# Optimization experiments

Measured on AMD Instinct MI355X. Metric: run time of the kernel, lower is better.

Reference implementation:

```python
import jax, jax.numpy as jnp
import numpy as np

MAX_WAVELENGTH = 10000.0
BIG_NEG = -2.3819763e+38
NUM_KV_HEADS = 8
HEAD_DIM = 128


def _apply_rope(x, positions):
    # x: [B, L, H, D], positions: [B, L]
    d = x.shape[-1]
    freq_exponents = (2.0 / d) * jnp.arange(d // 2, dtype=jnp.float32)
    timescale = MAX_WAVELENGTH ** freq_exponents                      # [D/2]
    radians = positions.astype(jnp.float32)[..., None] / timescale    # [B, L, D/2]
    radians = radians[..., None, :]                                   # [B, L, 1, D/2]
    sin, cos = jnp.sin(radians), jnp.cos(radians)
    x1, x2 = jnp.split(x, 2, axis=-1)
    return jnp.concatenate([x1 * cos - x2 * sin, x2 * cos + x1 * sin], axis=-1)


def setup_inputs() -> dict:
    key = jax.random.key(0)
    ks = jax.random.split(key, 4)
    B, T, D = 2, 2048, 4096
    N, K, H = 32, NUM_KV_HEADS, HEAD_DIM
    x = jax.random.normal(ks[0], (B, T, D), dtype=jnp.float32)
    positions = jnp.broadcast_to(jnp.arange(T, dtype=jnp.int32), (B, T))
    # causal mask [B, 1, T, S]
    attn_mask = jnp.broadcast_to(jnp.tril(jnp.ones((T, T), dtype=bool))[None, None], (B, 1, T, T))
    scale = 1.0 / np.sqrt(D)
    wq = jax.random.normal(ks[1], (N, D, H), dtype=jnp.float32) * scale
    wkv = jax.random.normal(ks[2], (2, K, D, H), dtype=jnp.float32) * scale
    wo = jax.random.normal(ks[3], (N, H, D), dtype=jnp.float32) * (1.0 / np.sqrt(N * H))
    return {"x": x, "positions": positions, "attn_mask": attn_mask,
            "wq": wq, "wkv": wkv, "wo": wo, "decode": 0}


def reference(x, positions, attn_mask, wq, wkv, wo, decode):
    # decode=False (prefill); KV cache path not exercised.
    B, T, D = x.shape
    N, _, H = wq.shape
    K = wkv.shape[1]
    G = N // K

    q = jnp.einsum('BTD,NDH->BTNH', x, wq)        # [B, T, N, H]
    k, v = jnp.einsum('BSD,2KDH->2BSKH', x, wkv)  # each [B, S, K, H]

    q = _apply_rope(q, positions) * (H ** -0.5)
    k = _apply_rope(k, positions)

    q = q.reshape(B, T, K, G, H)                  # 'B T (K G) H -> B T K G H'
    logits = jnp.einsum('BTKGH,BSKH->BKGTS', q, k).astype(jnp.float32)
    masked = jnp.where(attn_mask[:, :, None, :, :], logits, BIG_NEG)
    probs = jax.nn.softmax(masked, axis=-1).astype(k.dtype)
    encoded = jnp.einsum('BKGTS,BSKH->BTKGH', probs, v)
    encoded = encoded.reshape(B, T, N, H)
    return jnp.einsum('BTNH,NHD->BTD', encoded, wo)
```

## Files before the change

kernel.cpp:

```cpp
#include <hip/hip_runtime.h>

typedef short short8  __attribute__((ext_vector_type(8)));
typedef short short4v __attribute__((ext_vector_type(4)));
typedef float f32x4   __attribute__((ext_vector_type(4)));

#define B_   2
#define T_   2048
#define D_   4096
#define N_   32
#define KH_  8
#define H_   128
#define BT_  (B_*T_)
#define NH_  (N_*H_)
#define NTK  64

__device__ __forceinline__ short f2bf(float f) {
    unsigned u = __float_as_uint(f);
    u += 0x7fffu + ((u >> 16) & 1u);
    return (short)(u >> 16);
}

__device__ __forceinline__ void gl_lds16(const short* g, short* l) {
    __builtin_amdgcn_global_load_lds(
        (const __attribute__((address_space(1))) void*)(g),
        (__attribute__((address_space(3))) void*)(l), 16, 0, 0);
}

__global__ __launch_bounds__(256) void cast_x_kernel(const float* __restrict__ in,
                                                     short* __restrict__ out) {
    const size_t i = ((size_t)blockIdx.x * 256 + threadIdx.x) * 8;
    float4 v0 = *reinterpret_cast<const float4*>(in + i);
    float4 v1 = *reinterpret_cast<const float4*>(in + i + 4);
    short8 s;
    s[0] = f2bf(v0.x); s[1] = f2bf(v0.y); s[2] = f2bf(v0.z); s[3] = f2bf(v0.w);
    s[4] = f2bf(v1.x); s[5] = f2bf(v1.y); s[6] = f2bf(v1.z); s[7] = f2bf(v1.w);
    *reinterpret_cast<short8*>(out + i) = s;
}

__global__ void transpose_cast_kernel(const float* __restrict__ in,
                                      short* __restrict__ out, int R, int C) {
    __shared__ float tile[32][33];
    const long long slice = blockIdx.z;
    in  += slice * (long long)R * C;
    out += slice * (long long)R * C;
    const int c0 = blockIdx.x * 32, r0 = blockIdx.y * 32;
    const int tx = threadIdx.x, ty = threadIdx.y;
#pragma unroll
    for (int i = 0; i < 4; i++) {
        int r = r0 + ty + i * 8;
        tile[ty + i * 8][tx] = in[(long long)r * C + c0 + tx];
    }
    __syncthreads();
#pragma unroll
    for (int i = 0; i < 4; i++) {
        int cc = c0 + ty + i * 8;
        out[(long long)cc * R + r0 + tx] = f2bf(tile[tx][ty + i * 8]);
    }
}


#define RD_A(cb, jm) {                                                          \
    const int rr_ = arow0 + (jm) * 16;                                          \
    a[jm][0] = *reinterpret_cast<const short8*>(&lds[cb][0][ah][rr_ * 64 + at0]); \
    a[jm][1] = *reinterpret_cast<const short8*>(&lds[cb][0][ah][rr_ * 64 + at1]); }

#define RD_B(cb, jn, jj) {                                                      \
    const int rb_ = (jn) * 16 + l15;                                            \
    b[jj][0] = *reinterpret_cast<const short8*>(&lds[cb][1][wc][rb_ * 64 + at0]); \
    b[jj][1] = *reinterpret_cast<const short8*>(&lds[cb][1][wc][rb_ * 64 + at1]); }

#define STAGE(ab, G, rowbase, sb, h, kt_) {                                     \
    int kt_c = (kt_); if (kt_c > NTK - 1) kt_c = NTK - 1;                       \
    const short* gsrc_ = (G) + (size_t)((rowbase) + (h) * 128 + srow) * 4096    \
                             + kt_c * 64 + sca * 8;                             \
    gl_lds16(gsrc_,            &lds[sb][ab][h][(2 * w) * 512]);                 \
    gl_lds16(gsrc_ + 8 * 4096, &lds[sb][ab][h][(2 * w) * 512 + 512]); }

#define MFMA_Q(JM0, JN0)                                                        \
    __builtin_amdgcn_s_setprio(1);                                              \
    _Pragma("unroll")                                                           \
    for (int jm_ = 0; jm_ < 2; ++jm_)                                           \
    _Pragma("unroll")                                                           \
    for (int jn_ = 0; jn_ < 4; ++jn_)                                           \
    _Pragma("unroll")                                                           \
    for (int ks_ = 0; ks_ < 2; ++ks_)                                           \
        acc[(JM0) + jm_][(JN0) + jn_] = __builtin_amdgcn_mfma_f32_16x16x32_bf16( \
            a[(JM0) + jm_][ks_], b[jn_][ks_], acc[(JM0) + jm_][(JN0) + jn_], 0, 0, 0); \
    __builtin_amdgcn_s_setprio(0);

#define GEMM8_PRO_AND_LOOP(Ap, Bp, m0, n0)                                      \
    f32x4 acc[4][8];                                                            \
    {const f32x4 z_ = {0.f,0.f,0.f,0.f};                                        \
    _Pragma("unroll") for (int jm_=0;jm_<4;++jm_)                               \
    _Pragma("unroll") for (int jn_=0;jn_<8;++jn_) acc[jm_][jn_]=z_;}            \
    short8 a[4][2], b[4][2];                                                    \
    STAGE(0, Ap, m0, 0, 0, 0); STAGE(0, Ap, m0, 0, 1, 0);                       \
    STAGE(1, Bp, n0, 0, 0, 0); STAGE(1, Bp, n0, 0, 1, 0);                       \
    STAGE(0, Ap, m0, 1, 0, 1); STAGE(0, Ap, m0, 1, 1, 1);                       \
    for (int i = 0; i < NTK / 2; ++i) {                                         \
        _Pragma("unroll")                                                       \
        for (int hf = 0; hf < 2; ++hf) {                                        \
            const int cb = hf, sbB = hf ^ 1;                                    \
            const int tB = 2 * i + 1 + hf;                                      \
            const int tA = 2 * i + 2 + hf;                                      \
                                                                        \
            asm volatile("s_waitcnt vmcnt(4)" ::: "memory");                    \
            __builtin_amdgcn_s_barrier();                                       \
            RD_A(cb, 0); RD_A(cb, 1);                                           \
            RD_B(cb, 0, 0); RD_B(cb, 1, 1); RD_B(cb, 2, 2); RD_B(cb, 3, 3);     \
            STAGE(1, Bp, n0, sbB, 0, tB);                                       \
            MFMA_Q(0, 0);                                                       \
                                                                        \
            __builtin_amdgcn_s_barrier();                                       \
            RD_A(cb, 2); RD_A(cb, 3);                                           \
            STAGE(1, Bp, n0, sbB, 1, tB);                                       \
            MFMA_Q(2, 0);                                                       \
                                                                        \
            __builtin_amdgcn_s_barrier();                                       \
            RD_B(cb, 4, 0); RD_B(cb, 5, 1); RD_B(cb, 6, 2); RD_B(cb, 7, 3);     \
            STAGE(0, Ap, m0, hf, 0, tA);                                        \
            MFMA_Q(2, 4);                                                       \
                                                                        \
            __builtin_amdgcn_s_barrier();                                       \
            STAGE(0, Ap, m0, hf, 1, tA);                                        \
            MFMA_Q(0, 4);                                                       \
        }                                                                       \
    }                                                                           \
    asm volatile("s_waitcnt vmcnt(0)" ::: "memory");

__global__ __launch_bounds__(512, 2) void qkv_gemm8_kernel(
    const short* __restrict__ xb, const int* __restrict__ positions,
    const short* __restrict__ wqt,
    short* __restrict__ qo, short* __restrict__ ko, short* __restrict__ vto)
{
    __shared__ short lds[2][2][2][8192];
    const int tid = threadIdx.x;
    const int w = tid >> 6, lane = tid & 63;
    const int quad = lane >> 4, l15 = lane & 15;
    const int wr = w >> 1, wc = w & 1;
    const int ah = wr >> 1;
    const int arow0 = (wr & 1) * 64 + l15;
    const int sw = l15 & 7;
    const int at0 = (quad ^ sw) * 8;
    const int at1 = ((4 + quad) ^ sw) * 8;
    const int srow = 16 * w + (lane >> 3);
    const int sca = (lane & 7) ^ (lane >> 3);
    const int m0 = blockIdx.y * 256;
    const int n0 = blockIdx.x * 256;

    GEMM8_PRO_AND_LOOP(xb, wqt, m0, n0)

    const int head = 2 * blockIdx.x + wc;
    if (head < 40) {
        const float qs = (head < 32) ? (0.08838834764831845f * 1.4426950408889634f) : 1.0f;
#pragma unroll
        for (int jm = 0; jm < 4; ++jm) {
#pragma unroll
            for (int reg = 0; reg < 4; ++reg) {
                const int bt = m0 + wr * 64 + jm * 16 + quad * 4 + reg;
                const int bb = bt >> 11, t = bt & (T_ - 1);
                short* dst = (head < 32)
                    ? qo + ((size_t)(bb * N_ + head) * T_ + t) * H_
                    : ko + ((size_t)(bb * KH_ + (head - 32)) * T_ + t) * H_;
                const float pos = (float)positions[bt];
#pragma unroll
                for (int jn = 0; jn < 4; ++jn) {
                    const int h2 = jn * 16 + l15;
                    float inv_ts = exp2f((float)h2 * -0.20762050593048935f);
                    float rev = pos * inv_ts * 0.15915494309189535f;
                    rev -= floorf(rev);
                    float sn, cs;
                    __sincosf(rev * 6.283185307179586f, &sn, &cs);
                    float x1 = acc[jm][jn][reg], x2 = acc[jm][jn + 4][reg];
                    dst[h2]      = f2bf((x1 * cs - x2 * sn) * qs);
                    dst[h2 + 64] = f2bf((x2 * cs + x1 * sn) * qs);
                }
            }
        }
    } else {
        const int vh = head - 40;
        const int bb = m0 >> 11;
        const int tl0 = (m0 & (T_ - 1)) + wr * 64;
#pragma unroll
        for (int jm = 0; jm < 4; ++jm) {
            const int t0r = tl0 + jm * 16 + quad * 4;
#pragma unroll
            for (int jn = 0; jn < 8; ++jn) {
                const int h = jn * 16 + l15;
                short4v pv;
                pv[0] = f2bf(acc[jm][jn][0]); pv[1] = f2bf(acc[jm][jn][1]);
                pv[2] = f2bf(acc[jm][jn][2]); pv[3] = f2bf(acc[jm][jn][3]);
                *reinterpret_cast<short4v*>(vto + ((size_t)(bb * KH_ + vh) * H_ + h) * T_ + t0r) = pv;
            }
        }
    }
}

__global__ __launch_bounds__(512, 2) void out_gemm8_kernel(
    const short* __restrict__ enc, const short* __restrict__ wot,
    float* __restrict__ out)
{
    __shared__ short lds[2][2][2][8192];
    const int tid = threadIdx.x;
    const int w = tid >> 6, lane = tid & 63;
    const int quad = lane >> 4, l15 = lane & 15;
    const int wr = w >> 1, wc = w & 1;
    const int ah = wr >> 1;
    const int arow0 = (wr & 1) * 64 + l15;
    const int sw = l15 & 7;
    const int at0 = (quad ^ sw) * 8;
    const int at1 = ((4 + quad) ^ sw) * 8;
    const int srow = 16 * w + (lane >> 3);
    const int sca = (lane & 7) ^ (lane >> 3);
    const int m0 = blockIdx.y * 256;
    const int n0 = blockIdx.x * 256;

    GEMM8_PRO_AND_LOOP(enc, wot, m0, n0)

#pragma unroll
    for (int jm = 0; jm < 4; ++jm)
#pragma unroll
        for (int jn = 0; jn < 8; ++jn)
#pragma unroll
            for (int reg = 0; reg < 4; ++reg) {
                const int r = m0 + wr * 64 + jm * 16 + quad * 4 + reg;
                out[(size_t)r * D_ + n0 + wc * 128 + jn * 16 + l15] = acc[jm][jn][reg];
            }
}

__global__ __launch_bounds__(256) void attn_kernel(
    const short* __restrict__ qp, const short* __restrict__ kp,
    const short* __restrict__ vtp, short* __restrict__ encp)
{
    __shared__ short ldsP[4 * 32 * 128];
    const int tid = threadIdx.x;
    const int w = tid >> 6, lane = tid & 63;
    const int quad = lane >> 4, l15 = lane & 15;
    const int widx = blockIdx.x * 4 + w;
    const int pr = widx & 31;
    const int n  = (widx >> 5) & 31;
    const int b  = widx >> 10;
    const int kh = n >> 2;
    short* P = ldsP + w * (32 * 128);

    const short* qbase = qp  + (size_t)(b * N_  + n)  * T_ * H_;
    const short* kbase = kp  + (size_t)(b * KH_ + kh) * T_ * H_;
    const short* vbase = vtp + (size_t)(b * KH_ + kh) * H_ * T_;

    const f32x4 zero4 = {0.f, 0.f, 0.f, 0.f};

    for (int half = 0; half < 2; half++) {
        const int wt = half ? pr : (63 - pr);
        const int t0 = wt * 32;

        short8 qf[2][4];
#pragma unroll
        for (int jc = 0; jc < 2; jc++)
#pragma unroll
            for (int ks = 0; ks < 4; ks++)
                qf[jc][ks] = *reinterpret_cast<const short8*>(
                    qbase + (size_t)(t0 + 16 * jc + l15) * H_ + ks * 32 + quad * 8);

        f32x4 o[2][8];
#pragma unroll
        for (int jm = 0; jm < 2; jm++)
#pragma unroll
            for (int jn = 0; jn < 8; jn++) o[jm][jn] = zero4;
        float lsum[2] = {0.f, 0.f};

        short8 kb[8];
        short8 vb[8];
#pragma unroll
        for (int jn = 0; jn < 8; jn++)
            vb[jn] = *reinterpret_cast<const short8*>(
                vbase + (size_t)(16 * jn + l15) * T_ + quad * 8);
#pragma unroll
        for (int ks = 0; ks < 4; ks++)
#pragma unroll
            for (int jr = 0; jr < 2; jr++)
                kb[2 * ks + jr] = *reinterpret_cast<const short8*>(
                    kbase + (size_t)(16 * jr + l15) * H_ + ks * 32 + quad * 8);

        for (int ss = 0; ss <= wt; ss++) {
            const int s0 = ss * 32;
            const int slot = (ss & 3) * 4;
            const int s0n = (ss < wt) ? s0 + 32 : 0;

            f32x4 s[2][2];
#pragma unroll
            for (int jr = 0; jr < 2; jr++)
#pragma unroll
                for (int jc = 0; jc < 2; jc++) s[jr][jc] = zero4;
#pragma unroll
            for (int ks = 0; ks < 4; ks++)
#pragma unroll
                for (int jr = 0; jr < 2; jr++)
#pragma unroll
                    for (int jc = 0; jc < 2; jc++)
                        s[jr][jc] = __builtin_amdgcn_mfma_f32_16x16x32_bf16(kb[2 * ks + jr], qf[jc][ks], s[jr][jc], 0, 0, 0);

#pragma unroll
            for (int ks = 0; ks < 4; ks++)
#pragma unroll
                for (int jr = 0; jr < 2; jr++)
                    kb[2 * ks + jr] = *reinterpret_cast<const short8*>(
                        kbase + (size_t)(s0n + 16 * jr + l15) * H_ + ks * 32 + quad * 8);

            if (ss == wt) {
#pragma unroll
                for (int jr = 0; jr < 2; jr++)
#pragma unroll
                    for (int jc = 0; jc < 2; jc++)
#pragma unroll
                        for (int reg = 0; reg < 4; reg++) {
                            int sl = 16 * jr + 4 * quad + reg;
                            int tl = 16 * jc + l15;
                            if (sl > tl) s[jr][jc][reg] = -1.0e30f;
                        }
            }

#pragma unroll
            for (int jr = 0; jr < 2; jr++)
#pragma unroll
                for (int jc = 0; jc < 2; jc++) {
                    short4v pk;
#pragma unroll
                    for (int reg = 0; reg < 4; reg++) {
                        float p = exp2f(s[jr][jc][reg]);
                        lsum[jc] += p;
                        pk[reg] = f2bf(p);
                    }
                    const int row = 16 * jc + l15;
                    const int cc  = slot + 2 * jr + (quad >> 1);
                    const int hf  = quad & 1;
                    *reinterpret_cast<short4v*>(
                        &P[row * 128 + ((cc ^ l15) << 3) + (hf << 2)]) = pk;
                }
            asm volatile("s_waitcnt lgkmcnt(0)" ::: "memory");

#pragma unroll
            for (int jm = 0; jm < 2; jm++) {
                short8 pa = *reinterpret_cast<const short8*>(
                    &P[(16 * jm + l15) * 128 + (((slot + quad) ^ l15) << 3)]);
#pragma unroll
                for (int jn = 0; jn < 8; jn++)
                    o[jm][jn] = __builtin_amdgcn_mfma_f32_16x16x32_bf16(pa, vb[jn], o[jm][jn], 0, 0, 0);
            }

#pragma unroll
            for (int jn = 0; jn < 8; jn++)
                vb[jn] = *reinterpret_cast<const short8*>(
                    vbase + (size_t)(16 * jn + l15) * T_ + s0n + quad * 8);
        }

#pragma unroll
        for (int jc = 0; jc < 2; jc++) {
            lsum[jc] += __shfl_xor(lsum[jc], 16, 64);
            lsum[jc] += __shfl_xor(lsum[jc], 32, 64);
        }
#pragma unroll
        for (int jm = 0; jm < 2; jm++)
#pragma unroll
            for (int reg = 0; reg < 4; reg++) {
                const float inv = 1.0f / __shfl(lsum[jm], 4 * quad + reg, 64);
                const int t = t0 + 16 * jm + 4 * quad + reg;
                const size_t base = (size_t)(b * T_ + t) * NH_ + n * H_;
#pragma unroll
                for (int jn = 0; jn < 8; jn++)
                    encp[base + 16 * jn + l15] = f2bf(o[jm][jn][reg] * inv);
            }
    }
}

extern "C" void kernel_launch(void* const* d_in, const int* in_sizes, int n_in,
                              void* d_out, int out_size, void* d_ws, size_t ws_size,
                              hipStream_t stream)
{
    const float* x         = (const float*)d_in[0];
    const int*   positions = (const int*)d_in[1];
    const float* wq        = (const float*)d_in[3];
    const float* wkv       = (const float*)d_in[4];
    const float* wo        = (const float*)d_in[5];
    float* out = (float*)d_out;

    char* ws = (char*)d_ws;
    short* wqt  = (short*)(ws);
    short* wkvt = (short*)(ws + 33554432);
    short* q    = (short*)(ws + 50331648);
    short* kx   = (short*)(ws + 83886080);
    short* vt   = (short*)(ws + 92274688);
    short* xbf  = (short*)(ws + 100663296);
    short* wot  = (short*)(ws + 100663296);
    short* enc  = (short*)(ws);

    dim3 tb(32, 8);
    cast_x_kernel<<<dim3((BT_ * (size_t)D_) / 2048), dim3(256), 0, stream>>>(x, xbf);
    transpose_cast_kernel<<<dim3(H_/32, D_/32, N_),    tb, 0, stream>>>(wq,  wqt,  D_,  H_);
    transpose_cast_kernel<<<dim3(H_/32, D_/32, 2*KH_), tb, 0, stream>>>(wkv, wkvt, D_,  H_);

    qkv_gemm8_kernel<<<dim3(24, 16), dim3(512), 0, stream>>>(xbf, positions, wqt, q, kx, vt);

    transpose_cast_kernel<<<dim3(D_/32, NH_/32, 1),    tb, 0, stream>>>(wo,  wot,  NH_, D_);

    attn_kernel<<<dim3(512), dim3(256), 0, stream>>>(q, kx, vt, enc);

    out_gemm8_kernel<<<dim3(16, 16), dim3(512), 0, stream>>>(enc, wot, out);
}
```

Measured before the change: 788.7 us.

## Retile GEMMs to 256x128 with triple-buffered LDS and split attention KV loop

Both GEMM kernels move from 256x256 tiles with double-buffered LDS to 256x128 tiles with a three-stage LDS ring, one barrier per k-step, and a swizzled 1D block order for L2 locality. This doubles the block count so more work fits across CUs. The attention kernel splits each query block's KV loop across two waves, merges their partial outputs and sums through LDS, and drops the register prefetch of K/V. The trade is smaller tiles with more global reloads, plus extra syncthreads and LDS traffic in attention.

```diff
diff --git a/kernel.cpp b/kernel.cpp
--- a/kernel.cpp
+++ b/kernel.cpp
@@ -59,98 +59,91 @@
 }
 
 
-#define RD_A(cb, jm) {                                                          \
-    const int rr_ = arow0 + (jm) * 16;                                          \
-    a[jm][0] = *reinterpret_cast<const short8*>(&lds[cb][0][ah][rr_ * 64 + at0]); \
-    a[jm][1] = *reinterpret_cast<const short8*>(&lds[cb][0][ah][rr_ * 64 + at1]); }
-
-#define RD_B(cb, jn, jj) {                                                      \
-    const int rb_ = (jn) * 16 + l15;                                            \
-    b[jj][0] = *reinterpret_cast<const short8*>(&lds[cb][1][wc][rb_ * 64 + at0]); \
-    b[jj][1] = *reinterpret_cast<const short8*>(&lds[cb][1][wc][rb_ * 64 + at1]); }
-
-#define STAGE(ab, G, rowbase, sb, h, kt_) {                                     \
-    int kt_c = (kt_); if (kt_c > NTK - 1) kt_c = NTK - 1;                       \
-    const short* gsrc_ = (G) + (size_t)((rowbase) + (h) * 128 + srow) * 4096    \
-                             + kt_c * 64 + sca * 8;                             \
-    gl_lds16(gsrc_,            &lds[sb][ab][h][(2 * w) * 512]);                 \
-    gl_lds16(gsrc_ + 8 * 4096, &lds[sb][ab][h][(2 * w) * 512 + 512]); }
-
-#define MFMA_Q(JM0, JN0)                                                        \
+#define RA(cb, jm) {                                                            \
+    const int rr_ = arl + (jm) * 16 + l15;                                      \
+    a[jm][0] = *reinterpret_cast<const short8*>(&lds[cb][au][rr_ * 64 + at0]);  \
+    a[jm][1] = *reinterpret_cast<const short8*>(&lds[cb][au][rr_ * 64 + at1]); }
+
+#define RB(cb, jn) {                                                            \
+    const int rb_ = ((jn) >> 1) * 64 + wc * 32 + ((jn) & 1) * 16 + l15;         \
+    b[jn][0] = *reinterpret_cast<const short8*>(&lds[cb][2][rb_ * 64 + at0]);   \
+    b[jn][1] = *reinterpret_cast<const short8*>(&lds[cb][2][rb_ * 64 + at1]); }
+
+#define STG(G, grow, sb, un, kt_) {                                             \
+    int ktc_ = (kt_); if (ktc_ > NTK - 1) ktc_ = NTK - 1;                       \
+    const short* gs_ = (G) + (size_t)((grow) + srow) * 4096 + ktc_ * 64 + sca * 8; \
+    gl_lds16(gs_,            &lds[sb][un][(2 * w) * 512]);                      \
+    gl_lds16(gs_ + 8 * 4096, &lds[sb][un][(2 * w) * 512 + 512]); }
+
+#define MG(JM0, JN0)                                                            \
     __builtin_amdgcn_s_setprio(1);                                              \
     _Pragma("unroll")                                                           \
     for (int jm_ = 0; jm_ < 2; ++jm_)                                           \
     _Pragma("unroll")                                                           \
-    for (int jn_ = 0; jn_ < 4; ++jn_)                                           \
+    for (int jn_ = 0; jn_ < 2; ++jn_)                                           \
     _Pragma("unroll")                                                           \
     for (int ks_ = 0; ks_ < 2; ++ks_)                                           \
         acc[(JM0) + jm_][(JN0) + jn_] = __builtin_amdgcn_mfma_f32_16x16x32_bf16( \
-            a[(JM0) + jm_][ks_], b[jn_][ks_], acc[(JM0) + jm_][(JN0) + jn_], 0, 0, 0); \
+            a[(JM0) + jm_][ks_], b[(JN0) + jn_][ks_], acc[(JM0) + jm_][(JN0) + jn_], 0, 0, 0); \
     __builtin_amdgcn_s_setprio(0);
 
-#define GEMM8_PRO_AND_LOOP(Ap, Bp, m0, n0)                                      \
-    f32x4 acc[4][8];                                                            \
-    {const f32x4 z_ = {0.f,0.f,0.f,0.f};                                        \
-    _Pragma("unroll") for (int jm_=0;jm_<4;++jm_)                               \
-    _Pragma("unroll") for (int jn_=0;jn_<8;++jn_) acc[jm_][jn_]=z_;}            \
+#define GCORE(Ap, Bp, M0, N0)                                                   \
+    f32x4 acc[4][4];                                                            \
+    { const f32x4 z_ = {0.f, 0.f, 0.f, 0.f};                                    \
+      _Pragma("unroll") for (int i_ = 0; i_ < 4; ++i_)                          \
+      _Pragma("unroll") for (int j_ = 0; j_ < 4; ++j_) acc[i_][j_] = z_; }      \
     short8 a[4][2], b[4][2];                                                    \
-    STAGE(0, Ap, m0, 0, 0, 0); STAGE(0, Ap, m0, 0, 1, 0);                       \
-    STAGE(1, Bp, n0, 0, 0, 0); STAGE(1, Bp, n0, 0, 1, 0);                       \
-    STAGE(0, Ap, m0, 1, 0, 1); STAGE(0, Ap, m0, 1, 1, 1);                       \
-    for (int i = 0; i < NTK / 2; ++i) {                                         \
-        _Pragma("unroll")                                                       \
-        for (int hf = 0; hf < 2; ++hf) {                                        \
-            const int cb = hf, sbB = hf ^ 1;                                    \
-            const int tB = 2 * i + 1 + hf;                                      \
-            const int tA = 2 * i + 2 + hf;                                      \
-                                                                        \
-            asm volatile("s_waitcnt vmcnt(4)" ::: "memory");                    \
-            __builtin_amdgcn_s_barrier();                                       \
-            RD_A(cb, 0); RD_A(cb, 1);                                           \
-            RD_B(cb, 0, 0); RD_B(cb, 1, 1); RD_B(cb, 2, 2); RD_B(cb, 3, 3);     \
-            STAGE(1, Bp, n0, sbB, 0, tB);                                       \
-            MFMA_Q(0, 0);                                                       \
-                                                                        \
-            __builtin_amdgcn_s_barrier();                                       \
-            RD_A(cb, 2); RD_A(cb, 3);                                           \
-            STAGE(1, Bp, n0, sbB, 1, tB);                                       \
-            MFMA_Q(2, 0);                                                       \
-                                                                        \
-            __builtin_amdgcn_s_barrier();                                       \
-            RD_B(cb, 4, 0); RD_B(cb, 5, 1); RD_B(cb, 6, 2); RD_B(cb, 7, 3);     \
-            STAGE(0, Ap, m0, hf, 0, tA);                                        \
-            MFMA_Q(2, 4);                                                       \
-                                                                        \
-            __builtin_amdgcn_s_barrier();                                       \
-            STAGE(0, Ap, m0, hf, 1, tA);                                        \
-            MFMA_Q(0, 4);                                                       \
-        }                                                                       \
+    STG(Ap, (M0),       0, 0, 0); STG(Ap, (M0) + 128, 0, 1, 0);                 \
+    STG(Bp, (N0),       0, 2, 0);                                               \
+    STG(Ap, (M0),       1, 0, 1); STG(Ap, (M0) + 128, 1, 1, 1);                 \
+    STG(Bp, (N0),       1, 2, 1);                                               \
+    asm volatile("s_waitcnt vmcnt(6)" ::: "memory");                            \
+    __builtin_amdgcn_s_barrier();                                               \
+    for (int t = 0; t < NTK; ++t) {                                             \
+        const int cb = t % 3, pb = (t + 2) % 3;                                 \
+        RA(cb, 0); RA(cb, 1); RB(cb, 0); RB(cb, 1);                             \
+        STG(Ap, (M0), pb, 0, t + 2);                                            \
+        MG(0, 0);                                                               \
+        RA(cb, 2); RA(cb, 3);                                                   \
+        STG(Ap, (M0) + 128, pb, 1, t + 2);                                      \
+        MG(2, 0);                                                               \
+        RB(cb, 2); RB(cb, 3);                                                   \
+        STG(Bp, (N0), pb, 2, t + 2);                                            \
+        MG(2, 2);                                                               \
+        MG(0, 2);                                                               \
+        asm volatile("s_waitcnt vmcnt(6)" ::: "memory");                        \
+        __builtin_amdgcn_s_barrier();                                           \
     }                                                                           \
     asm volatile("s_waitcnt vmcnt(0)" ::: "memory");
+
+#define GEMM_PREAMBLE                                                           \
+    const int tid = threadIdx.x;                                                \
+    const int w = tid >> 6, lane = tid & 63;                                    \
+    const int quad = lane >> 4, l15 = lane & 15;                                \
+    const int wr = w >> 1, wc = w & 1;                                          \
+    const int au = wr >> 1;                                                     \
+    const int arl = (wr & 1) * 64;                                              \
+    const int sw = l15 & 7;                                                     \
+    const int at0 = (quad ^ sw) * 8;                                            \
+    const int at1 = ((4 + quad) ^ sw) * 8;                                      \
+    const int srow = 16 * w + (lane >> 3);                                      \
+    const int sca = (lane & 7) ^ (lane >> 3);
 
 __global__ __launch_bounds__(512, 2) void qkv_gemm8_kernel(
     const short* __restrict__ xb, const int* __restrict__ positions,
     const short* __restrict__ wqt,
     short* __restrict__ qo, short* __restrict__ ko, short* __restrict__ vto)
 {
-    __shared__ short lds[2][2][2][8192];
-    const int tid = threadIdx.x;
-    const int w = tid >> 6, lane = tid & 63;
-    const int quad = lane >> 4, l15 = lane & 15;
-    const int wr = w >> 1, wc = w & 1;
-    const int ah = wr >> 1;
-    const int arow0 = (wr & 1) * 64 + l15;
-    const int sw = l15 & 7;
-    const int at0 = (quad ^ sw) * 8;
-    const int at1 = ((4 + quad) ^ sw) * 8;
-    const int srow = 16 * w + (lane >> 3);
-    const int sca = (lane & 7) ^ (lane >> 3);
-    const int m0 = blockIdx.y * 256;
-    const int n0 = blockIdx.x * 256;
-
-    GEMM8_PRO_AND_LOOP(xb, wqt, m0, n0)
-
-    const int head = 2 * blockIdx.x + wc;
+    __shared__ short lds[3][3][8192];
+    GEMM_PREAMBLE
+    const int bid = blockIdx.x;
+    const int swz = (bid & 7) * 96 + (bid >> 3);
+    const int mt = swz / 48, nt = swz - mt * 48;
+    const int m0 = mt * 256, n0 = nt * 128;
+
+    GCORE(xb, wqt, m0, n0)
+
+    const int head = nt;
     if (head < 40) {
         const float qs = (head < 32) ? (0.08838834764831845f * 1.4426950408889634f) : 1.0f;
 #pragma unroll
@@ -164,14 +157,14 @@
                     : ko + ((size_t)(bb * KH_ + (head - 32)) * T_ + t) * H_;
                 const float pos = (float)positions[bt];
 #pragma unroll
-                for (int jn = 0; jn < 4; ++jn) {
-                    const int h2 = jn * 16 + l15;
+                for (int j = 0; j < 2; ++j) {
+                    const int h2 = wc * 32 + j * 16 + l15;
                     float inv_ts = exp2f((float)h2 * -0.20762050593048935f);
                     float rev = pos * inv_ts * 0.15915494309189535f;
                     rev -= floorf(rev);
                     float sn, cs;
                     __sincosf(rev * 6.283185307179586f, &sn, &cs);
-                    float x1 = acc[jm][jn][reg], x2 = acc[jm][jn + 4][reg];
+                    float x1 = acc[jm][j][reg], x2 = acc[jm][j + 2][reg];
                     dst[h2]      = f2bf((x1 * cs - x2 * sn) * qs);
                     dst[h2 + 64] = f2bf((x2 * cs + x1 * sn) * qs);
                 }
@@ -185,8 +178,8 @@
         for (int jm = 0; jm < 4; ++jm) {
             const int t0r = tl0 + jm * 16 + quad * 4;
 #pragma unroll
-            for (int jn = 0; jn < 8; ++jn) {
-                const int h = jn * 16 + l15;
+            for (int jn = 0; jn < 4; ++jn) {
+                const int h = (jn >> 1) * 64 + wc * 32 + (jn & 1) * 16 + l15;
                 short4v pv;
                 pv[0] = f2bf(acc[jm][jn][0]); pv[1] = f2bf(acc[jm][jn][1]);
                 pv[2] = f2bf(acc[jm][jn][2]); pv[3] = f2bf(acc[jm][jn][3]);
@@ -200,48 +193,45 @@
     const short* __restrict__ enc, const short* __restrict__ wot,
     float* __restrict__ out)
 {
-    __shared__ short lds[2][2][2][8192];
+    __shared__ short lds[3][3][8192];
+    GEMM_PREAMBLE
+    const int bid = blockIdx.x;
+    const int swz = (bid & 7) * 64 + (bid >> 3);
+    const int mt = swz >> 5, nt = swz & 31;
+    const int m0 = mt * 256, n0 = nt * 128;
+
+    GCORE(enc, wot, m0, n0)
+
+#pragma unroll
+    for (int jm = 0; jm < 4; ++jm)
+#pragma unroll
+        for (int jn = 0; jn < 4; ++jn) {
+            const int col = n0 + (jn >> 1) * 64 + wc * 32 + (jn & 1) * 16 + l15;
+#pragma unroll
+            for (int reg = 0; reg < 4; ++reg) {
+                const int r = m0 + wr * 64 + jm * 16 + quad * 4 + reg;
+                out[(size_t)r * D_ + col] = acc[jm][jn][reg];
+            }
+        }
+}
+
+__global__ __launch_bounds__(256, 4) void attn_kernel(
+    const short* __restrict__ qp, const short* __restrict__ kp,
+    const short* __restrict__ vtp, short* __restrict__ encp)
+{
+    __shared__ __align__(16) short ldsP[4][32 * 128];
+    __shared__ float ldsL[2][2][64];
     const int tid = threadIdx.x;
     const int w = tid >> 6, lane = tid & 63;
     const int quad = lane >> 4, l15 = lane & 15;
-    const int wr = w >> 1, wc = w & 1;
-    const int ah = wr >> 1;
-    const int arow0 = (wr & 1) * 64 + l15;
-    const int sw = l15 & 7;
-    const int at0 = (quad ^ sw) * 8;
-    const int at1 = ((4 + quad) ^ sw) * 8;
-    const int srow = 16 * w + (lane >> 3);
-    const int sca = (lane & 7) ^ (lane >> 3);
-    const int m0 = blockIdx.y * 256;
-    const int n0 = blockIdx.x * 256;
-
-    GEMM8_PRO_AND_LOOP(enc, wot, m0, n0)
-
-#pragma unroll
-    for (int jm = 0; jm < 4; ++jm)
-#pragma unroll
-        for (int jn = 0; jn < 8; ++jn)
-#pragma unroll
-            for (int reg = 0; reg < 4; ++reg) {
-                const int r = m0 + wr * 64 + jm * 16 + quad * 4 + reg;
-                out[(size_t)r * D_ + n0 + wc * 128 + jn * 16 + l15] = acc[jm][jn][reg];
-            }
-}
-
-__global__ __launch_bounds__(256) void attn_kernel(
-    const short* __restrict__ qp, const short* __restrict__ kp,
-    const short* __restrict__ vtp, short* __restrict__ encp)
-{
-    __shared__ short ldsP[4 * 32 * 128];
-    const int tid = threadIdx.x;
-    const int w = tid >> 6, lane = tid & 63;
-    const int quad = lane >> 4, l15 = lane & 15;
-    const int widx = blockIdx.x * 4 + w;
-    const int pr = widx & 31;
-    const int n  = (widx >> 5) & 31;
-    const int b  = widx >> 10;
+    const int pairi = w >> 1, sub = w & 1;
+    const int widx2 = blockIdx.x * 2 + pairi;
+    const int pr = widx2 & 31;
+    const int n  = (widx2 >> 5) & 31;
+    const int b  = widx2 >> 10;
     const int kh = n >> 2;
-    short* P = ldsP + w * (32 * 128);
+    short* P = ldsP[w];
+    float* OC = reinterpret_cast<float*>(&ldsP[2 * pairi][0]);
 
     const short* qbase = qp  + (size_t)(b * N_  + n)  * T_ * H_;
     const short* kbase = kp  + (size_t)(b * KH_ + kh) * T_ * H_;
@@ -268,43 +258,34 @@
             for (int jn = 0; jn < 8; jn++) o[jm][jn] = zero4;
         float lsum[2] = {0.f, 0.f};
 
-        short8 kb[8];
-        short8 vb[8];
-#pragma unroll
-        for (int jn = 0; jn < 8; jn++)
-            vb[jn] = *reinterpret_cast<const short8*>(
-                vbase + (size_t)(16 * jn + l15) * T_ + quad * 8);
-#pragma unroll
-        for (int ks = 0; ks < 4; ks++)
+        for (int ss = sub; ss <= wt; ss += 2) {
+            const int s0 = ss * 32;
+            const int slot = ((ss >> 1) & 3) * 4;
+
+            short8 vb[8];
+#pragma unroll
+            for (int jn = 0; jn < 8; jn++)
+                vb[jn] = *reinterpret_cast<const short8*>(
+                    vbase + (size_t)(16 * jn + l15) * T_ + s0 + quad * 8);
+
+            f32x4 s[2][2];
 #pragma unroll
             for (int jr = 0; jr < 2; jr++)
-                kb[2 * ks + jr] = *reinterpret_cast<const short8*>(
-                    kbase + (size_t)(16 * jr + l15) * H_ + ks * 32 + quad * 8);
-
-        for (int ss = 0; ss <= wt; ss++) {
-            const int s0 = ss * 32;
-            const int slot = (ss & 3) * 4;
-            const int s0n = (ss < wt) ? s0 + 32 : 0;
-
-            f32x4 s[2][2];
-#pragma unroll
-            for (int jr = 0; jr < 2; jr++)
 #pragma unroll
                 for (int jc = 0; jc < 2; jc++) s[jr][jc] = zero4;
 #pragma unroll
-            for (int ks = 0; ks < 4; ks++)
+            for (int ks = 0; ks < 4; ks++) {
+                short8 kb[2];
 #pragma unroll
                 for (int jr = 0; jr < 2; jr++)
+                    kb[jr] = *reinterpret_cast<const short8*>(
+                        kbase + (size_t)(s0 + 16 * jr + l15) * H_ + ks * 32 + quad * 8);
+#pragma unroll
+                for (int jr = 0; jr < 2; jr++)
 #pragma unroll
                     for (int jc = 0; jc < 2; jc++)
-                        s[jr][jc] = __builtin_amdgcn_mfma_f32_16x16x32_bf16(kb[2 * ks + jr], qf[jc][ks], s[jr][jc], 0, 0, 0);
-
-#pragma unroll
-            for (int ks = 0; ks < 4; ks++)
-#pragma unroll
-                for (int jr = 0; jr < 2; jr++)
-                    kb[2 * ks + jr] = *reinterpret_cast<const short8*>(
-                        kbase + (size_t)(s0n + 16 * jr + l15) * H_ + ks * 32 + quad * 8);
+                        s[jr][jc] = __builtin_amdgcn_mfma_f32_16x16x32_bf16(kb[jr], qf[jc][ks], s[jr][jc], 0, 0, 0);
+            }
 
             if (ss == wt) {
 #pragma unroll
@@ -346,29 +327,48 @@
                 for (int jn = 0; jn < 8; jn++)
                     o[jm][jn] = __builtin_amdgcn_mfma_f32_16x16x32_bf16(pa, vb[jn], o[jm][jn], 0, 0, 0);
             }
-
-#pragma unroll
-            for (int jn = 0; jn < 8; jn++)
-                vb[jn] = *reinterpret_cast<const short8*>(
-                    vbase + (size_t)(16 * jn + l15) * T_ + s0n + quad * 8);
-        }
-
-#pragma unroll
-        for (int jc = 0; jc < 2; jc++) {
-            lsum[jc] += __shfl_xor(lsum[jc], 16, 64);
-            lsum[jc] += __shfl_xor(lsum[jc], 32, 64);
-        }
-#pragma unroll
-        for (int jm = 0; jm < 2; jm++)
-#pragma unroll
-            for (int reg = 0; reg < 4; reg++) {
-                const float inv = 1.0f / __shfl(lsum[jm], 4 * quad + reg, 64);
-                const int t = t0 + 16 * jm + 4 * quad + reg;
-                const size_t base = (size_t)(b * T_ + t) * NH_ + n * H_;
+        }
+
+        __syncthreads();
+        if (sub == 1) {
+#pragma unroll
+            for (int jm = 0; jm < 2; jm++)
 #pragma unroll
                 for (int jn = 0; jn < 8; jn++)
-                    encp[base + 16 * jn + l15] = f2bf(o[jm][jn][reg] * inv);
-            }
+                    *reinterpret_cast<f32x4*>(&OC[((jm * 8 + jn) * 64 + lane) * 4]) = o[jm][jn];
+            ldsL[pairi][0][lane] = lsum[0];
+            ldsL[pairi][1][lane] = lsum[1];
+        }
+        __syncthreads();
+        if (sub == 0) {
+#pragma unroll
+            for (int jm = 0; jm < 2; jm++)
+#pragma unroll
+                for (int jn = 0; jn < 8; jn++) {
+                    f32x4 t = *reinterpret_cast<const f32x4*>(&OC[((jm * 8 + jn) * 64 + lane) * 4]);
+                    o[jm][jn] += t;
+                }
+            lsum[0] += ldsL[pairi][0][lane];
+            lsum[1] += ldsL[pairi][1][lane];
+
+#pragma unroll
+            for (int jc = 0; jc < 2; jc++) {
+                lsum[jc] += __shfl_xor(lsum[jc], 16, 64);
+                lsum[jc] += __shfl_xor(lsum[jc], 32, 64);
+            }
+#pragma unroll
+            for (int jm = 0; jm < 2; jm++)
+#pragma unroll
+                for (int reg = 0; reg < 4; reg++) {
+                    const float inv = 1.0f / __shfl(lsum[jm], 4 * quad + reg, 64);
+                    const int t = t0 + 16 * jm + 4 * quad + reg;
+                    const size_t base = (size_t)(b * T_ + t) * NH_ + n * H_;
+#pragma unroll
+                    for (int jn = 0; jn < 8; jn++)
+                        encp[base + 16 * jn + l15] = f2bf(o[jm][jn][reg] * inv);
+                }
+        }
+        __syncthreads();
     }
 }
 
@@ -398,11 +398,11 @@
     transpose_cast_kernel<<<dim3(H_/32, D_/32, N_),    tb, 0, stream>>>(wq,  wqt,  D_,  H_);
     transpose_cast_kernel<<<dim3(H_/32, D_/32, 2*KH_), tb, 0, stream>>>(wkv, wkvt, D_,  H_);
 
-    qkv_gemm8_kernel<<<dim3(24, 16), dim3(512), 0, stream>>>(xbf, positions, wqt, q, kx, vt);
+    qkv_gemm8_kernel<<<dim3(768), dim3(512), 0, stream>>>(xbf, positions, wqt, q, kx, vt);
 
     transpose_cast_kernel<<<dim3(D_/32, NH_/32, 1),    tb, 0, stream>>>(wo,  wot,  NH_, D_);
 
-    attn_kernel<<<dim3(512), dim3(256), 0, stream>>>(q, kx, vt, enc);
-
-    out_gemm8_kernel<<<dim3(16, 16), dim3(512), 0, stream>>>(enc, wot, out);
-}
+    attn_kernel<<<dim3(1024), dim3(256), 0, stream>>>(q, kx, vt, enc);
+
+    out_gemm8_kernel<<<dim3(512), dim3(512), 0, stream>>>(enc, wot, out);
+}
```

Result: slower. 1.049 ms (+33.0%).
